# Kernel optimization log

Hardware: AMD Instinct MI355X
Metric: run time of the kernel (lower is better)

## Reference

```python
import jax, jax.numpy as jnp
import numpy as np

B, L, D_IN, D_GATE, D_HID, D_STATE = 4, 8192, 512, 2048, 128, 512
EPS = 1e-5


def _layernorm(x, g, b):
    m = jnp.mean(x, axis=-1, keepdims=True)
    v = jnp.var(x, axis=-1, keepdims=True)
    return (x - m) * jax.lax.rsqrt(v + EPS) * g + b


def _dss(u, g, b, lam_re, lam_im, c_re, c_im, d):
    # u: [B, L, H]; diagonal state-space mixing along L via FFT conv
    seq_len = u.shape[-2]
    un = _layernorm(u, g, b)
    residual = un * d                                   # learned skip, [B,L,H]
    lam = -jnp.exp(lam_re) + 1j * jnp.exp(lam_im)       # [N] complex
    c = (c_re + 1j * c_im) * (jnp.exp(lam) - 1.0) / lam  # [H,N]
    t = jnp.arange(seq_len, dtype=jnp.float32)
    s = jnp.exp(t[:, None] * lam[None, :])              # [L,N] Vandermonde
    kern = jnp.einsum('hn,ln->lh', c, s).real           # [L,H]
    n_fft = 2 * seq_len
    uf = jnp.fft.rfft(un, n=n_fft, axis=-2)             # [B, n_fft/2+1, H]
    kf = jnp.fft.rfft(kern, n=n_fft, axis=0)            # [n_fft/2+1, H]
    y = jnp.fft.irfft(uf * kf, n=n_fft, axis=-2)[..., :seq_len, :]
    return y + residual


def setup_inputs() -> dict:
    key = jax.random.key(0)
    ks = jax.random.split(key, 16)
    f32 = jnp.float32
    return {
        'x': jax.random.normal(ks[0], (B, L, D_IN), f32),
        'norm_g': jnp.ones((D_IN,), f32),
        'norm_b': jnp.zeros((D_IN,), f32),
        'W_v': jax.random.normal(ks[1], (D_GATE, D_IN), f32) / np.sqrt(D_IN),
        'W_u': jax.random.normal(ks[2], (D_HID, D_IN), f32) / np.sqrt(D_IN),
        'W_uc': jax.random.normal(ks[3], (D_GATE, D_HID), f32) / np.sqrt(D_HID),
        'W_o': jax.random.normal(ks[4], (D_IN, D_GATE), f32) / np.sqrt(D_GATE),
        'b_o': jnp.zeros((D_IN,), f32),
        'dss_g': jnp.ones((D_HID,), f32),
        'dss_b': jnp.zeros((D_HID,), f32),
        'lam_re': jax.random.normal(ks[5], (D_STATE,), f32),
        'lam_im': jax.random.normal(ks[6], (D_STATE,), f32),
        'C_re': jax.random.normal(ks[7], (D_HID, D_STATE), f32) / np.sqrt(D_STATE),
        'C_im': jax.random.normal(ks[8], (D_HID, D_STATE), f32) / np.sqrt(D_STATE),
        'D_skip': jax.random.normal(ks[9], (D_HID,), f32),
    }


def reference(x, norm_g, norm_b, W_v, W_u, W_uc, W_o, b_o,
              dss_g, dss_b, lam_re, lam_im, C_re, C_im, D_skip):
    xn = _layernorm(x, norm_g, norm_b)
    v = jax.nn.gelu(jnp.einsum('blf,gf->blg', xn, W_v), approximate=False)  # [B,L,G]
    u = jax.nn.gelu(jnp.einsum('blf,hf->blh', xn, W_u), approximate=False)  # [B,L,H]
    y = _dss(u, dss_g, dss_b, lam_re, lam_im, C_re, C_im, D_skip)           # [B,L,H]
    uc = jnp.einsum('blh,gh->blg', y, W_uc)                                 # [B,L,G]
    o = jnp.einsum('blg,fg->blf', uc * v, W_o) + b_o                        # [B,L,F]
    return o + x
```

## Files before the change

### kernel.cpp

```cpp
#include <hip/hip_runtime.h>
#include <math.h>
#include <stdint.h>

typedef unsigned short u16;
typedef unsigned int   u32;
typedef short short8 __attribute__((ext_vector_type(8)));
typedef float v4f    __attribute__((ext_vector_type(4)));

#define DEVI static __device__ __forceinline__

struct __align__(8)  U2 { u32 x, y; };
struct __align__(16) U4 { u32 x, y, z, w; };

static const int BB = 4, LL = 8192;
static const int BL = BB * LL;

DEVI float bf2f(u16 u){ u32 v = ((u32)u) << 16; float f; __builtin_memcpy(&f, &v, 4); return f; }
DEVI u16  f2bf(float f){ u32 u; __builtin_memcpy(&u, &f, 4); return (u16)((u + 0x7fffu + ((u >> 16) & 1u)) >> 16); }

DEVI float geluf(float x){
  float z = fabsf(x) * 0.7071067811865475f;
  float t = __builtin_amdgcn_rcpf(1.0f + 0.3275911f * z);
  float p = t * (0.254829592f + t * (-0.284496736f + t * (1.421413741f +
            t * (-1.453152027f + t * 1.061405429f))));
  float e = __builtin_amdgcn_exp2f(z * z * -1.4426950408889634f);
  float er = 1.0f - p * e;
  float s = (x < 0.0f) ? -er : er;
  return 0.5f * x * (1.0f + s);
}

DEVI void ldsload16(const void* g, void* l){
  __builtin_amdgcn_global_load_lds(
      (const __attribute__((address_space(1))) u32*)(uintptr_t)g,
      (__attribute__((address_space(3)))  u32*)(u32)(uintptr_t)l,
      16, 0, 0);
}

__global__ __launch_bounds__(256) void k_cvt4(
    const float* __restrict__ s0, u16* __restrict__ d0, int n0,
    const float* __restrict__ s1, u16* __restrict__ d1, int n1,
    const float* __restrict__ s2, u16* __restrict__ d2, int n2,
    const float* __restrict__ s3, u16* __restrict__ d3, int n3){
  int i = blockIdx.x * 256 + threadIdx.x;
  if (i < n0){ d0[i] = f2bf(s0[i]); return; }
  i -= n0;
  if (i < n1){ d1[i] = f2bf(s1[i]); return; }
  i -= n1;
  if (i < n2){ d2[i] = f2bf(s2[i]); return; }
  i -= n2;
  if (i < n3){ d3[i] = f2bf(s3[i]); }
}

__global__ __launch_bounds__(256) void k_ln1(const float* __restrict__ x, const float* __restrict__ g,
                                             const float* __restrict__ b, u16* __restrict__ xn){
  int row = blockIdx.x, t = threadIdx.x;
  const float2* xr = (const float2*)(x + (int64_t)row * 512);
  float2 p = xr[t];
  float s = p.x + p.y, ss = p.x * p.x + p.y * p.y;
  for (int off = 32; off; off >>= 1){ s += __shfl_down(s, off); ss += __shfl_down(ss, off); }
  __shared__ float red[8];
  int w = t >> 6, lane = t & 63;
  if (!lane){ red[w] = s; red[4 + w] = ss; }
  __syncthreads();
  s  = red[0] + red[1] + red[2] + red[3];
  ss = red[4] + red[5] + red[6] + red[7];
  float m = s * (1.0f / 512.0f), var = ss * (1.0f / 512.0f) - m * m;
  float rs = rsqrtf(var + 1e-5f);
  float2 gv = ((const float2*)g)[t], bv = ((const float2*)b)[t];
  float r0 = (p.x - m) * rs * gv.x + bv.x;
  float r1 = (p.y - m) * rs * gv.y + bv.y;
  ((u32*)(xn + (int64_t)row * 512))[t] = (u32)f2bf(r0) | ((u32)f2bf(r1) << 16);
}

__global__ __launch_bounds__(256) void k_ln2(const u16* __restrict__ u, const float* __restrict__ g,
                                             const float* __restrict__ b, u16* __restrict__ un){
  int row = blockIdx.x * 4 + (threadIdx.x >> 6);
  int lane = threadIdx.x & 63;
  const u32* ur = (const u32*)(u + (int64_t)row * 128);
  u32 pv = ur[lane];
  float a = bf2f((u16)(pv & 0xffff)), c = bf2f((u16)(pv >> 16));
  float s = a + c, ss = a * a + c * c;
  for (int off = 32; off; off >>= 1){ s += __shfl_xor(s, off); ss += __shfl_xor(ss, off); }
  float m = s * (1.0f / 128.0f), var = ss * (1.0f / 128.0f) - m * m;
  float rs = rsqrtf(var + 1e-5f);
  float2 gv = ((const float2*)g)[lane], bv = ((const float2*)b)[lane];
  float r0 = (a - m) * rs * gv.x + bv.x;
  float r1 = (c - m) * rs * gv.y + bv.y;
  ((u32*)(un + (int64_t)row * 128))[lane] = (u32)f2bf(r0) | ((u32)f2bf(r1) << 16);
}

__global__ __launch_bounds__(256) void k_transpose(const u16* __restrict__ un, u16* __restrict__ unT){
  int bc = blockIdx.x >> 3, it = blockIdx.x & 7;
  int b = bc >> 4, cc = bc & 15;
  __shared__ __align__(16) u16 tile[64][128];
  const u16* src = un + ((int64_t)(b * 8192 + cc * 512 + it * 64)) * 128;
  int t = threadIdx.x;
  for (int p = 0; p < 4; p++){
    int id = p * 256 + t; int ri = id >> 4, seg = id & 15;
    *(U4*)&tile[ri][seg * 8] = *(const U4*)(src + (int64_t)ri * 128 + seg * 8);
  }
  __syncthreads();
  u16* dst = unT + ((int64_t)(bc * 128)) * 512 + it * 64;
  for (int p = 0; p < 4; p++){
    int id = p * 256 + t; int h = id >> 3, seg = id & 7;
    U4 pk; u16* pv = (u16*)&pk;
    for (int k2 = 0; k2 < 8; k2++) pv[k2] = tile[seg * 8 + k2][h];
    *(U4*)(dst + (int64_t)h * 512 + seg * 8) = pk;
  }
}

__global__ __launch_bounds__(512) void k_prep(const float* lam_re, const float* lam_im,
    const float* C_re, const float* C_im,
    u16* ZC, u16* PC, u16* VC, u16* ccat, float* cre, float* cim, float* zT){
  int n = blockIdx.x, t = threadIdx.x;
  float lr = -expf(lam_re[n]);
  float li =  expf(lam_im[n]);
  float mag = expf(lr * (float)t), ph = li * (float)t;
  float er = mag * cosf(ph), ei = mag * sinf(ph);
  ZC[(int64_t)n * 512 + (511 - t)]         = f2bf(er);
  ZC[(int64_t)(512 + n) * 512 + (511 - t)] = f2bf(ei);
  VC[(int64_t)t * 1024 + n]       = f2bf(er);
  VC[(int64_t)t * 1024 + 512 + n] = f2bf(-ei);
  float mag2 = expf(lr * (float)(t + 1)), ph2 = li * (float)(t + 1);
  PC[(int64_t)t * 1024 + n]       = f2bf(mag2 * cosf(ph2));
  PC[(int64_t)t * 1024 + 512 + n] = f2bf(-mag2 * sinf(ph2));
  if (t == 0){
    float m5 = expf(lr * 512.0f), p5 = li * 512.0f;
    zT[n] = m5 * cosf(p5); zT[512 + n] = m5 * sinf(p5);
  }
  if (t < 128){
    float e1m = expf(lr);
    float e1r = e1m * cosf(li), e1i = e1m * sinf(li);
    float nr = e1r - 1.0f, ni = e1i;
    float d2 = lr * lr + li * li;
    float qr = (nr * lr + ni * li) / d2, qi = (ni * lr - nr * li) / d2;
    float Cr = C_re[t * 512 + n], Ci = C_im[t * 512 + n];
    float vr = Cr * qr - Ci * qi, vi = Cr * qi + Ci * qr;
    cre[t * 512 + n] = vr; cim[t * 512 + n] = vi;
    ccat[(int64_t)t * 1024 + n] = f2bf(vr); ccat[(int64_t)t * 1024 + 512 + n] = f2bf(vi);
  }
}

__global__ __launch_bounds__(128) void k_kern(const u16* __restrict__ VC,
                                              const u16* __restrict__ ccat,
                                              float* __restrict__ kern){
  __shared__ __align__(16) u16 vrow[1024];
  int d = blockIdx.x, h = threadIdx.x;
  *(U4*)&vrow[h * 8] = *(const U4*)(VC + (int64_t)d * 1024 + h * 8);
  __syncthreads();
  const u16* cr = ccat + (int64_t)h * 1024;
  float s = 0.0f;
  #pragma unroll 4
  for (int k = 0; k < 1024; k += 8){
    short8 a = *(const short8*)&vrow[k];
    short8 b = *(const short8*)(cr + k);
    #pragma unroll
    for (int j = 0; j < 8; j++) s += bf2f((u16)a[j]) * bf2f((u16)b[j]);
  }
  kern[(int64_t)d * 128 + h] = s;
}

__global__ __launch_bounds__(512) void k_rcat(const float* __restrict__ kern, u16* __restrict__ Rcat){
  int h = blockIdx.x >> 7, a = blockIdx.x & 127;
  int kcol = threadIdx.x;
  int d = 3 - (kcol >> 7);
  int delay = d * 128 + a - (kcol & 127);
  float val = (delay >= 0 && delay < 512) ? kern[delay * 128 + h] : 0.0f;
  Rcat[((int64_t)(h * 128 + a)) * 512 + kcol] = f2bf(val);
}

__global__ __launch_bounds__(256) void k_scan(const float* __restrict__ S, const float* __restrict__ cre,
    const float* __restrict__ cim, const float* __restrict__ zT, u16* __restrict__ WT){
  int tid = blockIdx.x * 256 + threadIdx.x;
  int n = tid & 511, bh = tid >> 9, b = bh >> 7, h = bh & 127;
  float cr = cre[h * 512 + n], ci = cim[h * 512 + n];
  float zr = zT[n], zi = zT[512 + n];
  float sR = 0.0f, sI = 0.0f;
  for (int cc = 0; cc < 16; cc++){
    int64_t m = (int64_t)(b * 16 + cc) * 128 + h;
    float wR = cr * sR - ci * sI, wI = cr * sI + ci * sR;
    WT[m * 1024 + n] = f2bf(wR);
    WT[m * 1024 + 512 + n] = f2bf(wI);
    float aR = S[m * 1024 + n], aI = S[m * 1024 + 512 + n];
    float nR = zr * sR - zi * sI + aR;
    sI = zr * sI + zi * sR + aI;
    sR = nR;
  }
}

__global__ __launch_bounds__(256) void k_assemble(const float* __restrict__ Yloc, const float* __restrict__ Ycross,
    const u16* __restrict__ un, const float* __restrict__ Dskip, u16* __restrict__ y){
  int64_t e = (int64_t)blockIdx.x * 256 + threadIdx.x;
  int h = (int)(e & 127); int64_t bl = e >> 7;
  int b = (int)(bl >> 13), l = (int)(bl & 8191);
  int cc = l >> 9, ii = l & 511, bc = b * 16 + cc;
  float val = Yloc[((int64_t)h * 512 + ii) * 64 + bc]
            + Ycross[(int64_t)ii * 8192 + (int64_t)bc * 128 + h]
            + bf2f(un[e]) * Dskip[h];
  y[e] = f2bf(val);
}

template<int EPI, bool TRI = false>
__global__ __launch_bounds__(256) void k_gemm(
    const u16* __restrict__ A, int64_t lda, int64_t aZ,
    const u16* __restrict__ B, int64_t ldb, int64_t bZ,
    void* Cp, int64_t ldc, int64_t cZ,
    int K, int Nvalid,
    const u16* aux1, const float* auxf1, const float* auxf2)
{
  __shared__ union __align__(16) SMU { u16 st[2][4096]; float ep[4][1088]; } sm;
  const int tid = threadIdx.x;
  const int lane = tid & 63, w = tid >> 6;
  const int wr = w >> 1, wc = w & 1, q = lane >> 4, c16 = lane & 15;
  const int sRow = lane >> 2, sSeg = lane & 3;
  const int z = blockIdx.z;

  int bx = blockIdx.x, by = blockIdx.y;
  if (!TRI && (gridDim.y & 7) == 0 && gridDim.x > 1){
    u32 idx = by * gridDim.x + bx;
    u32 xcd = idx & 7, s = idx >> 3;
    bx = s % gridDim.x;
    by = (s / gridDim.x) * 8 + xcd;
  }
  const int64_t m0 = (int64_t)by * 128;
  const int64_t n0 = (int64_t)bx * 128;

  const u16* Ab = A + (int64_t)z * aZ;
  const u16* Bp = B + (int64_t)z * bZ;
  int Keff = K;
  if (TRI){
    Ab += 384 - m0;
    Keff = (int)(m0 + 128);
  }

  v4f acc[4][4];
  #pragma unroll
  for (int i = 0; i < 4; i++)
    #pragma unroll
    for (int j = 0; j < 4; j++)
      acc[i][j] = (v4f)0.0f;

  for (int k0 = 0; k0 < Keff; k0 += 32){
    #pragma unroll
    for (int half = 0; half < 2; half++){
      int r0 = (half * 4 + w) * 16;
      int64_t arow = (TRI ? (int64_t)0 : m0) + r0 + sRow;
      ldsload16(Ab + arow * lda + k0 + sSeg * 8, &sm.st[0][r0 * 32]);
      int64_t brow = n0 + r0 + sRow;
      if (brow >= Nvalid) brow = Nvalid - 1;
      ldsload16(Bp + brow * ldb + k0 + sSeg * 8, &sm.st[1][r0 * 32]);
    }
    __syncthreads();
    short8 af[4], bfr[4];
    const u16* aB = &sm.st[0][(wr * 64 + c16) * 32 + q * 8];
    const u16* bB = &sm.st[1][(wc * 64 + c16) * 32 + q * 8];
    #pragma unroll
    for (int i = 0; i < 4; i++) af[i]  = *(const short8*)(aB + i * 512);
    #pragma unroll
    for (int j = 0; j < 4; j++) bfr[j] = *(const short8*)(bB + j * 512);
    #pragma unroll
    for (int i = 0; i < 4; i++)
      #pragma unroll
      for (int j = 0; j < 4; j++)
        acc[i][j] = __builtin_amdgcn_mfma_f32_16x16x32_bf16(af[i], bfr[j], acc[i][j], 0, 0, 0);
    __syncthreads();
  }

  if (EPI == 0){
    float* Cf = (float*)Cp + (int64_t)z * cZ;
    #pragma unroll
    for (int i = 0; i < 4; i++)
      #pragma unroll
      for (int j = 0; j < 4; j++){
        int64_t gr = m0 + wr * 64 + i * 16 + q * 4;
        int64_t gc = n0 + wc * 64 + j * 16 + c16;
        if (gc < Nvalid){
          #pragma unroll
          for (int r = 0; r < 4; r++)
            Cf[(gr + r) * ldc + gc] = acc[i][j][r];
        }
      }
    return;
  }

  u16* Cb = (u16*)Cp + (int64_t)z * cZ;
  float* ep = sm.ep[w];
  for (int i = 0; i < 4; i++){
    #pragma unroll
    for (int j = 0; j < 4; j++)
      #pragma unroll
      for (int r = 0; r < 4; r++){
        float vv = acc[i][j][r];
        if (EPI == 1) vv = geluf(vv);
        ep[(q * 4 + r) * 68 + j * 16 + c16] = vv;
      }
    #pragma unroll
    for (int p = 0; p < 4; p++){
      int id = p * 64 + lane;
      int row = id >> 4, cg = id & 15;
      float o0 = ep[row * 68 + cg * 4 + 0];
      float o1 = ep[row * 68 + cg * 4 + 1];
      float o2 = ep[row * 68 + cg * 4 + 2];
      float o3 = ep[row * 68 + cg * 4 + 3];
      int64_t gr = m0 + wr * 64 + i * 16 + row;
      int64_t gc = n0 + wc * 64 + cg * 4;
      if (gc < Nvalid){
        U2 outp;
        outp.x = (u32)f2bf(o0) | ((u32)f2bf(o1) << 16);
        outp.y = (u32)f2bf(o2) | ((u32)f2bf(o3) << 16);
        *(U2*)(Cb + gr * ldc + gc) = outp;
      }
    }
  }
}

#define FENCE __builtin_amdgcn_sched_barrier(0)
#define BARX  __builtin_amdgcn_s_barrier()

#define STAGE(SRC, LD, TBASE, SEL, KT)                                          \
  { const u16* _g = (SRC) + (int64_t)(KT) * 64 + (int64_t)((SEL) * 128 + wid * 8) * (LD); \
    u16* _lb = (TBASE) + ((SEL) * 128 + wid * 8) * 64;                          \
    ldsload16(_g, _lb);                                                         \
    ldsload16(_g + (int64_t)64 * (LD), _lb + 64 * 64);                          \
  }

#define MFMAQ(QM, QN, BQ)                                                       \
  __builtin_amdgcn_s_setprio(1);                                                \
  _Pragma("unroll")                                                             \
  for (int mi = 0; mi < 4; mi++)                                                \
    _Pragma("unroll")                                                           \
    for (int ni = 0; ni < 2; ni++){                                             \
      acc[(QM)*4+mi][(QN)*2+ni] = __builtin_amdgcn_mfma_f32_16x16x32_bf16(      \
          af[mi][0], BQ[ni][0], acc[(QM)*4+mi][(QN)*2+ni], 0, 0, 0);            \
      acc[(QM)*4+mi][(QN)*2+ni] = __builtin_amdgcn_mfma_f32_16x16x32_bf16(      \
          af[mi][1], BQ[ni][1], acc[(QM)*4+mi][(QN)*2+ni], 0, 0, 0);            \
    }                                                                           \
  __builtin_amdgcn_s_setprio(0);

#define DS_READ_A(OFF)                                                          \
    _Pragma("unroll")                                                           \
    for (int mi = 0; mi < 4; mi++){                                             \
      af[mi][0] = *(const short8*)(Ac + (OFF) + abase + mi * 2048 + kx0);       \
      af[mi][1] = *(const short8*)(Ac + (OFF) + abase + mi * 2048 + kx1);       \
    }
#define DS_READ_B(BQ, OFF)                                                      \
    _Pragma("unroll")                                                           \
    for (int ni = 0; ni < 2; ni++){                                             \
      BQ[ni][0] = *(const short8*)(Bc + (OFF) + bbase + ni * 2048 + kx0);       \
      BQ[ni][1] = *(const short8*)(Bc + (OFF) + bbase + ni * 2048 + kx1);       \
    }

#define DO_TILE(T, CURB, NXTB)                                                  \
  {                                                                             \
    const char* Ac = (const char*)(CURB);                                       \
    const char* Bc = Ac + 32768;                                                \
    if ((T) + 1 < NT){                                                          \
      u16* Ab_ = (NXTB); u16* Bb_ = (NXTB) + 16384;                             \
      STAGE(Asrc, lda, Ab_, 0, (T) + 1);                                        \
      STAGE(Asrc, lda, Ab_, 1, (T) + 1);                                        \
      STAGE(Bsrc, ldb, Bb_, 0, (T) + 1);                                        \
      STAGE(Bsrc, ldb, Bb_, 1, (T) + 1);                                        \
    }                                                                           \
    DS_READ_A(0) DS_READ_B(bq0, 0) DS_READ_B(bq1, 16384)                        \
    MFMAQ(0, 0, bq0);                                                           \
    MFMAQ(0, 1, bq1);                                                           \
    DS_READ_A(16384)                                                            \
    MFMAQ(1, 1, bq1);                                                           \
    MFMAQ(1, 0, bq0);                                                           \
    asm volatile("s_waitcnt lgkmcnt(0)" ::: "memory");                          \
    if ((T) + 1 < NT) asm volatile("s_waitcnt vmcnt(0)" ::: "memory");          \
    FENCE; BARX; FENCE;                                                         \
  }

template<int EPI>
__global__ __launch_bounds__(512) void k_gemm256(
    const u16* __restrict__ A, int64_t lda,
    const u16* __restrict__ B, int64_t ldb,
    void* __restrict__ Cp, int64_t ldc, int K,
    const u16* __restrict__ aux1,
    const float* __restrict__ auxf1, const float* __restrict__ auxf2)
{
  extern __shared__ __align__(16) u16 smd[];
  const int tid = threadIdx.x, wid = tid >> 6, lane = tid & 63;
  const int wr = wid >> 2, wc = wid & 3, c16 = lane & 15;
  const int q4 = (lane >> 4) << 2;

  int bx = blockIdx.x, by = blockIdx.y;
  if ((gridDim.y & 7) == 0 && gridDim.x > 1){
    u32 idx = by * gridDim.x + bx;
    u32 xcd = idx & 7, s = idx >> 3;
    bx = s % gridDim.x;
    by = (s / gridDim.x) * 8 + xcd;
  }
  const int64_t m0 = (int64_t)by * 256;
  const int64_t n0 = (int64_t)bx * 256;
  const int NT = K >> 6;

  const int rowin = lane >> 3;
  const int colel = 8 * ((lane & 7) ^ rowin);
  const u16* Asrc = A + (m0 + rowin) * lda + colel;
  const u16* Bsrc = B + (n0 + rowin) * ldb + colel;

  const int kx0 = ((lane >> 4) << 4) ^ ((lane & 7) << 4);
  const int kx1 = kx0 ^ 64;
  const int abase = (wr * 64 + c16) * 128;
  const int bbase = (wc * 32 + c16) * 128;

  u16* buf0 = smd;
  u16* buf1 = smd + 32768;

  v4f acc[8][4];
  #pragma unroll
  for (int i = 0; i < 8; i++)
    #pragma unroll
    for (int j = 0; j < 4; j++) acc[i][j] = (v4f)0.0f;

  short8 af[4][2], bq0[2][2], bq1[2][2];

  STAGE(Asrc, lda, buf0,         0, 0);
  STAGE(Asrc, lda, buf0,         1, 0);
  STAGE(Bsrc, ldb, buf0 + 16384, 0, 0);
  STAGE(Bsrc, ldb, buf0 + 16384, 1, 0);
  asm volatile("s_waitcnt vmcnt(0)" ::: "memory");
  FENCE; BARX; FENCE;

  for (int t = 0; t < NT; t += 2){
    DO_TILE(t,     buf0, buf1)
    DO_TILE(t + 1, buf1, buf0)
  }

  if (EPI == 0){
    float* C = (float*)Cp;
    #pragma unroll
    for (int qm = 0; qm < 2; qm++)
      #pragma unroll
      for (int mi = 0; mi < 4; mi++){
        int64_t gr = m0 + qm * 128 + wr * 64 + mi * 16 + q4;
        #pragma unroll
        for (int qn = 0; qn < 2; qn++)
          #pragma unroll
          for (int ni = 0; ni < 2; ni++){
            int64_t gc = n0 + qn * 128 + wc * 32 + ni * 16 + c16;
            v4f a = acc[qm * 4 + mi][qn * 2 + ni];
            float bo = auxf2[gc];
            #pragma unroll
            for (int r = 0; r < 4; r++)
              C[(gr + r) * ldc + gc] = a[r] + auxf1[(gr + r) * ldc + gc] + bo;
          }
      }
    return;
  }

  u16* Cb = (u16*)Cp;
  float* scr = (float*)smd + wid * 528;
  const int erow = lane >> 2, eseg = lane & 3;
  #pragma unroll
  for (int qm = 0; qm < 2; qm++)
    #pragma unroll
    for (int mi = 0; mi < 4; mi++)
      #pragma unroll
      for (int qn = 0; qn < 2; qn++){
        #pragma unroll
        for (int ni = 0; ni < 2; ni++){
          v4f a = acc[qm * 4 + mi][qn * 2 + ni];
          #pragma unroll
          for (int r = 0; r < 4; r++){
            float vv = a[r];
            if (EPI == 1) vv = geluf(vv);
            scr[(q4 + r) * 33 + ni * 16 + c16] = vv;
          }
        }
        float o[8];
        #pragma unroll
        for (int kq = 0; kq < 8; kq++) o[kq] = scr[erow * 33 + eseg * 8 + kq];
        int64_t gr = m0 + qm * 128 + wr * 64 + mi * 16 + erow;
        int64_t gc = n0 + qn * 128 + wc * 32 + eseg * 8;
        if (EPI == 2){
          U4 pv = *(const U4*)(aux1 + gr * ldc + gc);
          const u16* pp = (const u16*)&pv;
          #pragma unroll
          for (int kq = 0; kq < 8; kq++) o[kq] *= bf2f(pp[kq]);
        }
        U4 outp; u16* op = (u16*)&outp;
        #pragma unroll
        for (int kq = 0; kq < 8; kq++) op[kq] = f2bf(o[kq]);
        *(U4*)(Cb + gr * ldc + gc) = outp;
      }
}

extern "C" void kernel_launch(void* const* d_in, const int* in_sizes, int n_in,
                              void* d_out, int out_size, void* d_ws, size_t ws_size,
                              hipStream_t stream) {
  (void)in_sizes; (void)n_in; (void)out_size; (void)ws_size;
  const float* x      = (const float*)d_in[0];
  const float* norm_g = (const float*)d_in[1];
  const float* norm_b = (const float*)d_in[2];
  const float* W_v    = (const float*)d_in[3];
  const float* W_u    = (const float*)d_in[4];
  const float* W_uc   = (const float*)d_in[5];
  const float* W_o    = (const float*)d_in[6];
  const float* b_o    = (const float*)d_in[7];
  const float* dss_g  = (const float*)d_in[8];
  const float* dss_b  = (const float*)d_in[9];
  const float* lam_re = (const float*)d_in[10];
  const float* lam_im = (const float*)d_in[11];
  const float* C_re   = (const float*)d_in[12];
  const float* C_im   = (const float*)d_in[13];
  const float* D_skip = (const float*)d_in[14];

  char* ob = (char*)d_out;
  u16* xn    = (u16*)(ob);
  u16* Wv_b  = (u16*)(ob + 33554432ull);
  u16* Wu_b  = (u16*)(ob + 35651584ull);

  char* ws = (char*)d_ws;
  const size_t R1      = 134217728ull;
  const size_t OFF_UN  = R1 + 33554432ull;
  const size_t OFF_UNT = OFF_UN + 8388608ull;
  const size_t OFF_R2  = OFF_UNT + 8388608ull;
  const size_t OFF_TAB = OFF_R2 + 33554432ull;

  u16*  v     = (u16*)(ws + 0);
  u16*  u     = (u16*)(ws + R1);
  u16*  Rcat  = (u16*)(ws + R1);
  u16*  WT    = (u16*)(ws + R1 + 16777216ull);
  u16*  un    = (u16*)(ws + OFF_UN);
  u16*  unT   = (u16*)(ws + OFF_UNT);
  u16*  y     = (u16*)(ws + OFF_UNT);
  float* S    = (float*)(ws + OFF_R2);
  float* Ycross = (float*)(ws + OFF_R2);
  float* Yloc = (float*)(ws + OFF_R2 + 16777216ull);
  char* tp = ws + OFF_TAB;
  u16*  ZC   = (u16*)tp;            tp += 1048576;
  u16*  PC   = (u16*)tp;            tp += 1048576;
  u16*  VC   = (u16*)tp;            tp += 1048576;
  u16*  ccat = (u16*)tp;            tp += 262144;
  float* cre = (float*)tp;          tp += 262144;
  float* cim = (float*)tp;          tp += 262144;
  float* zT  = (float*)tp;          tp += 4096;
  float* kern= (float*)tp;          tp += 262144;
  u16*  Wo_b = (u16*)tp;            tp += 2097152;
  u16*  Wuc_b= (u16*)tp;            tp += 524288;

  k_cvt4<<<9472, 256, 0, stream>>>(W_v, Wv_b, 2048 * 512,
                                   W_u, Wu_b, 128 * 512,
                                   W_uc, Wuc_b, 2048 * 128,
                                   W_o, Wo_b, 512 * 2048);

  k_ln1<<<BL, 256, 0, stream>>>(x, norm_g, norm_b, xn);
  k_prep<<<512, 512, 0, stream>>>(lam_re, lam_im, C_re, C_im, ZC, PC, VC, ccat, cre, cim, zT);
  k_kern<<<512, 128, 0, stream>>>(VC, ccat, kern);

  k_gemm256<1><<<dim3(8, 128), 512, 131072, stream>>>(xn, 512, Wv_b, 512, v, 2048, 512, nullptr, nullptr, nullptr);
  k_gemm<1><<<dim3(1, 256, 1), 256, 0, stream>>>(xn, 512, 0, Wu_b, 512, 0, u, 128, 0, 512, 128, nullptr, nullptr, nullptr);
  k_ln2<<<BL / 4, 256, 0, stream>>>(u, dss_g, dss_b, un);
  k_transpose<<<512, 256, 0, stream>>>(un, unT);

  k_rcat<<<16384, 512, 0, stream>>>(kern, Rcat);

  k_gemm<0><<<dim3(8, 64, 1), 256, 0, stream>>>(unT, 512, 0, ZC, 512, 0, S, 1024, 0, 512, 1024, nullptr, nullptr, nullptr);
  k_scan<<<1024, 256, 0, stream>>>(S, cre, cim, zT, WT);
  k_gemm<0><<<dim3(64, 4, 1), 256, 0, stream>>>(PC, 1024, 0, WT, 1024, 0, Ycross, 8192, 0, 1024, 8192, nullptr, nullptr, nullptr);
  k_gemm<0, true><<<dim3(1, 4, 128), 256, 0, stream>>>(
      Rcat, 512, 65536, unT, 65536, 512, Yloc, 64, 32768, 512, 64, nullptr, nullptr, nullptr);
  k_assemble<<<16384, 256, 0, stream>>>(Yloc, Ycross, un, D_skip, y);

  k_gemm256<2><<<dim3(8, 128), 512, 131072, stream>>>(y, 128, Wuc_b, 128, v, 2048, 128, v, nullptr, nullptr);
  k_gemm256<0><<<dim3(2, 128), 512, 131072, stream>>>(v, 2048, Wo_b, 2048, d_out, 512, 2048, nullptr, x, b_o);
}
```

Measured before the change: 596.3 us.

## Add K=128 gate GEMM kernel keeping A tile resident; tile assemble transpose

```diff
diff --git a/kernel.cpp b/kernel.cpp
--- a/kernel.cpp
+++ b/kernel.cpp
@@ -188,16 +188,33 @@
   }
 }
 
-__global__ __launch_bounds__(256) void k_assemble(const float* __restrict__ Yloc, const float* __restrict__ Ycross,
-    const u16* __restrict__ un, const float* __restrict__ Dskip, u16* __restrict__ y){
-  int64_t e = (int64_t)blockIdx.x * 256 + threadIdx.x;
-  int h = (int)(e & 127); int64_t bl = e >> 7;
-  int b = (int)(bl >> 13), l = (int)(bl & 8191);
-  int cc = l >> 9, ii = l & 511, bc = b * 16 + cc;
-  float val = Yloc[((int64_t)h * 512 + ii) * 64 + bc]
-            + Ycross[(int64_t)ii * 8192 + (int64_t)bc * 128 + h]
-            + bf2f(un[e]) * Dskip[h];
-  y[e] = f2bf(val);
+__global__ __launch_bounds__(512) void k_assemble2(const float* __restrict__ Yloc,
+    const float* __restrict__ Ycross, const u16* __restrict__ un,
+    const float* __restrict__ Dskip, u16* __restrict__ y){
+  __shared__ float tile[128][65];
+  int ii = blockIdx.x;
+  int t = threadIdx.x;
+  int hl = t >> 6;
+  int bcl = t & 63;
+  #pragma unroll
+  for (int p = 0; p < 16; p++){
+    int h = p * 8 + hl;
+    tile[h][bcl] = Yloc[((int64_t)(h * 512 + ii)) * 64 + bcl];
+  }
+  __syncthreads();
+  int h = t & 127;
+  int bcr = t >> 7;
+  float dk = Dskip[h];
+  #pragma unroll
+  for (int p = 0; p < 16; p++){
+    int bc = p * 4 + bcr;
+    int b = bc >> 4, cc = bc & 15;
+    int64_t e = ((int64_t)b * 8192 + cc * 512 + ii) * 128 + h;
+    float val = tile[h][bc]
+              + Ycross[(int64_t)ii * 8192 + (int64_t)bc * 128 + h]
+              + bf2f(un[e]) * dk;
+    y[e] = f2bf(val);
+  }
 }
 
 template<int EPI, bool TRI = false>
@@ -475,17 +492,144 @@
         for (int kq = 0; kq < 8; kq++) o[kq] = scr[erow * 33 + eseg * 8 + kq];
         int64_t gr = m0 + qm * 128 + wr * 64 + mi * 16 + erow;
         int64_t gc = n0 + qn * 128 + wc * 32 + eseg * 8;
-        if (EPI == 2){
-          U4 pv = *(const U4*)(aux1 + gr * ldc + gc);
-          const u16* pp = (const u16*)&pv;
-          #pragma unroll
-          for (int kq = 0; kq < 8; kq++) o[kq] *= bf2f(pp[kq]);
-        }
         U4 outp; u16* op = (u16*)&outp;
         #pragma unroll
         for (int kq = 0; kq < 8; kq++) op[kq] = f2bf(o[kq]);
         *(U4*)(Cb + gr * ldc + gc) = outp;
       }
+}
+
+__global__ __launch_bounds__(512) void k_gemmK128(
+    const u16* __restrict__ A,
+    const u16* __restrict__ B,
+    u16* __restrict__ C)
+{
+  extern __shared__ __align__(16) u16 smd[];
+  const int tid = threadIdx.x, wid = tid >> 6, lane = tid & 63;
+  const int wr = wid >> 2, wc = wid & 3, c16 = lane & 15;
+  const int q4 = (lane >> 4) << 2;
+
+  int bx = blockIdx.x, by = blockIdx.y;
+  {
+    u32 idx = by * gridDim.x + bx;
+    u32 xcd = idx & 7, s = idx >> 3;
+    bx = s % gridDim.x;
+    by = (s / gridDim.x) * 8 + xcd;
+  }
+  const int64_t m0 = (int64_t)by * 256;
+  const int64_t nbase = (int64_t)bx * 1024;
+
+  const int rowin = lane >> 3;
+  const int colel = 8 * ((lane & 7) ^ rowin);
+  const u16* Asrc = A + (m0 + rowin) * 128 + colel;
+
+  const int kx0 = ((lane >> 4) << 4) ^ ((lane & 7) << 4);
+  const int kx1 = kx0 ^ 64;
+  const int abase = (wr * 64 + c16) * 128;
+  const int bbase = (wc * 32 + c16) * 128;
+
+  u16* Abuf = smd;
+  u16* Bbuf = smd + 32768;
+  float* scr = (float*)(smd + 65536) + wid * 528;
+
+  const int erow = lane >> 2, eseg = lane & 3;
+  short8 af[4][2], bq0[2][2], bq1[2][2];
+
+  {
+    const u16* Bs0 = B + (nbase + rowin) * 128 + colel;
+    STAGE(Asrc, 128, Abuf,         0, 0);
+    STAGE(Asrc, 128, Abuf,         1, 0);
+    STAGE(Asrc, 128, Abuf + 16384, 0, 1);
+    STAGE(Asrc, 128, Abuf + 16384, 1, 1);
+    STAGE(Bs0,  128, Bbuf,         0, 0);
+    STAGE(Bs0,  128, Bbuf,         1, 0);
+    STAGE(Bs0,  128, Bbuf + 16384, 0, 1);
+    STAGE(Bs0,  128, Bbuf + 16384, 1, 1);
+  }
+  asm volatile("s_waitcnt vmcnt(0)" ::: "memory");
+  FENCE; BARX; FENCE;
+
+  #pragma unroll
+  for (int nj = 0; nj < 4; nj++){
+    const int64_t n0 = nbase + nj * 256;
+
+    v4f acc[8][4];
+    #pragma unroll
+    for (int i = 0; i < 8; i++)
+      #pragma unroll
+      for (int j = 0; j < 4; j++) acc[i][j] = (v4f)0.0f;
+
+    #pragma unroll
+    for (int kt = 0; kt < 2; kt++){
+      const char* Ac = (const char*)Abuf + kt * 32768;
+      const char* Bc = (const char*)Bbuf + kt * 32768;
+      DS_READ_A(0) DS_READ_B(bq0, 0) DS_READ_B(bq1, 16384)
+      MFMAQ(0, 0, bq0);
+      MFMAQ(0, 1, bq1);
+      DS_READ_A(16384)
+      MFMAQ(1, 1, bq1);
+      MFMAQ(1, 0, bq0);
+    }
+    asm volatile("s_waitcnt lgkmcnt(0)" ::: "memory");
+    FENCE; BARX; FENCE;
+
+    if (nj < 3){
+      const u16* Bs = B + (nbase + (nj + 1) * 256 + rowin) * 128 + colel;
+      STAGE(Bs, 128, Bbuf,         0, 0);
+      STAGE(Bs, 128, Bbuf,         1, 0);
+      STAGE(Bs, 128, Bbuf + 16384, 0, 1);
+      STAGE(Bs, 128, Bbuf + 16384, 1, 1);
+    }
+
+    U4 pvA[2], pvB[2];
+    {
+      int64_t gr = m0 + wr * 64 + erow;
+      pvA[0] = *(const U4*)(C + gr * 2048 + n0 + wc * 32 + eseg * 8);
+      pvA[1] = *(const U4*)(C + gr * 2048 + n0 + 128 + wc * 32 + eseg * 8);
+    }
+    #pragma unroll
+    for (int g = 0; g < 8; g++){
+      const int qm = g >> 2, mi = g & 3;
+      int64_t gr0 = m0 + qm * 128 + wr * 64 + mi * 16;
+      if (g < 7){
+        const int qn2 = (g + 1) >> 2, mn2 = (g + 1) & 3;
+        int64_t gr2 = m0 + qn2 * 128 + wr * 64 + mn2 * 16 + erow;
+        if (g & 1){
+          pvA[0] = *(const U4*)(C + gr2 * 2048 + n0 + wc * 32 + eseg * 8);
+          pvA[1] = *(const U4*)(C + gr2 * 2048 + n0 + 128 + wc * 32 + eseg * 8);
+        } else {
+          pvB[0] = *(const U4*)(C + gr2 * 2048 + n0 + wc * 32 + eseg * 8);
+          pvB[1] = *(const U4*)(C + gr2 * 2048 + n0 + 128 + wc * 32 + eseg * 8);
+        }
+      }
+      #pragma unroll
+      for (int qn = 0; qn < 2; qn++){
+        #pragma unroll
+        for (int ni = 0; ni < 2; ni++){
+          v4f a = acc[qm * 4 + mi][qn * 2 + ni];
+          #pragma unroll
+          for (int r = 0; r < 4; r++)
+            scr[(q4 + r) * 33 + ni * 16 + c16] = a[r];
+        }
+        float o[8];
+        #pragma unroll
+        for (int kq = 0; kq < 8; kq++) o[kq] = scr[erow * 33 + eseg * 8 + kq];
+        U4 pv = (g & 1) ? pvB[qn] : pvA[qn];
+        const u16* pp = (const u16*)&pv;
+        U4 outp; u16* op = (u16*)&outp;
+        #pragma unroll
+        for (int kq = 0; kq < 8; kq++) op[kq] = f2bf(o[kq] * bf2f(pp[kq]));
+        int64_t gr = gr0 + erow;
+        int64_t gc = n0 + qn * 128 + wc * 32 + eseg * 8;
+        *(U4*)(C + gr * 2048 + gc) = outp;
+      }
+    }
+
+    if (nj < 3){
+      asm volatile("s_waitcnt vmcnt(0)" ::: "memory");
+      FENCE; BARX; FENCE;
+    }
+  }
 }
 
 extern "C" void kernel_launch(void* const* d_in, const int* in_sizes, int n_in,
@@ -563,8 +707,8 @@
   k_gemm<0><<<dim3(64, 4, 1), 256, 0, stream>>>(PC, 1024, 0, WT, 1024, 0, Ycross, 8192, 0, 1024, 8192, nullptr, nullptr, nullptr);
   k_gemm<0, true><<<dim3(1, 4, 128), 256, 0, stream>>>(
       Rcat, 512, 65536, unT, 65536, 512, Yloc, 64, 32768, 512, 64, nullptr, nullptr, nullptr);
-  k_assemble<<<16384, 256, 0, stream>>>(Yloc, Ycross, un, D_skip, y);
-
-  k_gemm256<2><<<dim3(8, 128), 512, 131072, stream>>>(y, 128, Wuc_b, 128, v, 2048, 128, v, nullptr, nullptr);
+  k_assemble2<<<512, 512, 0, stream>>>(Yloc, Ycross, un, D_skip, y);
+
+  k_gemmK128<<<dim3(2, 128), 512, 148480, stream>>>(y, Wuc_b, v);
   k_gemm256<0><<<dim3(2, 128), 512, 131072, stream>>>(v, 2048, Wo_b, 2048, d_out, 512, 2048, nullptr, x, b_o);
 }
```

After: 611.5 us. 2.5% more time.

## Triple-buffer 256-tile GEMM with K=32 stages and tile the assemble transpose

Applied to the files above, without the earlier changes.

```diff
diff --git a/kernel.cpp b/kernel.cpp
--- a/kernel.cpp
+++ b/kernel.cpp
@@ -188,16 +188,33 @@
   }
 }
 
-__global__ __launch_bounds__(256) void k_assemble(const float* __restrict__ Yloc, const float* __restrict__ Ycross,
-    const u16* __restrict__ un, const float* __restrict__ Dskip, u16* __restrict__ y){
-  int64_t e = (int64_t)blockIdx.x * 256 + threadIdx.x;
-  int h = (int)(e & 127); int64_t bl = e >> 7;
-  int b = (int)(bl >> 13), l = (int)(bl & 8191);
-  int cc = l >> 9, ii = l & 511, bc = b * 16 + cc;
-  float val = Yloc[((int64_t)h * 512 + ii) * 64 + bc]
-            + Ycross[(int64_t)ii * 8192 + (int64_t)bc * 128 + h]
-            + bf2f(un[e]) * Dskip[h];
-  y[e] = f2bf(val);
+__global__ __launch_bounds__(512) void k_assemble2(const float* __restrict__ Yloc,
+    const float* __restrict__ Ycross, const u16* __restrict__ un,
+    const float* __restrict__ Dskip, u16* __restrict__ y){
+  __shared__ float tile[128][65];
+  int ii = blockIdx.x;
+  int t = threadIdx.x;
+  int hl = t >> 6;
+  int bcl = t & 63;
+  #pragma unroll
+  for (int p = 0; p < 16; p++){
+    int h = p * 8 + hl;
+    tile[h][bcl] = Yloc[((int64_t)(h * 512 + ii)) * 64 + bcl];
+  }
+  __syncthreads();
+  int h = t & 127;
+  int bcr = t >> 7;
+  float dk = Dskip[h];
+  #pragma unroll
+  for (int p = 0; p < 16; p++){
+    int bc = p * 4 + bcr;
+    int b = bc >> 4, cc = bc & 15;
+    int64_t e = ((int64_t)b * 8192 + cc * 512 + ii) * 128 + h;
+    float val = tile[h][bc]
+              + Ycross[(int64_t)ii * 8192 + (int64_t)bc * 128 + h]
+              + bf2f(un[e]) * dk;
+    y[e] = f2bf(val);
+  }
 }
 
 template<int EPI, bool TRI = false>
@@ -317,58 +334,38 @@
 #define FENCE __builtin_amdgcn_sched_barrier(0)
 #define BARX  __builtin_amdgcn_s_barrier()
 
-#define STAGE(SRC, LD, TBASE, SEL, KT)                                          \
-  { const u16* _g = (SRC) + (int64_t)(KT) * 64 + (int64_t)((SEL) * 128 + wid * 8) * (LD); \
-    u16* _lb = (TBASE) + ((SEL) * 128 + wid * 8) * 64;                          \
-    ldsload16(_g, _lb);                                                         \
-    ldsload16(_g + (int64_t)64 * (LD), _lb + 64 * 64);                          \
-  }
-
-#define MFMAQ(QM, QN, BQ)                                                       \
-  __builtin_amdgcn_s_setprio(1);                                                \
-  _Pragma("unroll")                                                             \
-  for (int mi = 0; mi < 4; mi++)                                                \
+#define STAGE32(SRC, LD, BUFO, OPO, SEL, KT)                                    \
+  { const u16* _g = (SRC) + (int64_t)(KT) * 32 + (int64_t)((SEL) * 128 + wid * 16) * (LD); \
+    u16* _lb = smd + (BUFO) + (OPO) + ((SEL) * 128 + wid * 16) * 32;            \
+    ldsload16(_g, _lb); }
+
+#define DO_T(T, CUR, FUT)                                                       \
+  {                                                                             \
+    if ((T) + 2 < NT){                                                          \
+      STAGE32(Asrc, lda, (FUT), 0,    0, (T) + 2);                              \
+      STAGE32(Asrc, lda, (FUT), 0,    1, (T) + 2);                              \
+      STAGE32(Bsrc, ldb, (FUT), 8192, 0, (T) + 2);                              \
+      STAGE32(Bsrc, ldb, (FUT), 8192, 1, (T) + 2);                              \
+    }                                                                           \
+    const char* Ac = (const char*)(smd + (CUR));                                \
+    const char* Bc = (const char*)(smd + (CUR) + 8192);                         \
     _Pragma("unroll")                                                           \
-    for (int ni = 0; ni < 2; ni++){                                             \
-      acc[(QM)*4+mi][(QN)*2+ni] = __builtin_amdgcn_mfma_f32_16x16x32_bf16(      \
-          af[mi][0], BQ[ni][0], acc[(QM)*4+mi][(QN)*2+ni], 0, 0, 0);            \
-      acc[(QM)*4+mi][(QN)*2+ni] = __builtin_amdgcn_mfma_f32_16x16x32_bf16(      \
-          af[mi][1], BQ[ni][1], acc[(QM)*4+mi][(QN)*2+ni], 0, 0, 0);            \
-    }                                                                           \
-  __builtin_amdgcn_s_setprio(0);
-
-#define DS_READ_A(OFF)                                                          \
+    for (int mi = 0; mi < 8; mi++)                                              \
+      af[mi] = *(const short8*)(Ac + abase + mi * 1024 + kx);                   \
     _Pragma("unroll")                                                           \
-    for (int mi = 0; mi < 4; mi++){                                             \
-      af[mi][0] = *(const short8*)(Ac + (OFF) + abase + mi * 2048 + kx0);       \
-      af[mi][1] = *(const short8*)(Ac + (OFF) + abase + mi * 2048 + kx1);       \
-    }
-#define DS_READ_B(BQ, OFF)                                                      \
+    for (int ni = 0; ni < 4; ni++)                                              \
+      bf[ni] = *(const short8*)(Bc + bbase + ni * 1024 + kx);                   \
+    __builtin_amdgcn_s_setprio(1);                                              \
     _Pragma("unroll")                                                           \
-    for (int ni = 0; ni < 2; ni++){                                             \
-      BQ[ni][0] = *(const short8*)(Bc + (OFF) + bbase + ni * 2048 + kx0);       \
-      BQ[ni][1] = *(const short8*)(Bc + (OFF) + bbase + ni * 2048 + kx1);       \
-    }
-
-#define DO_TILE(T, CURB, NXTB)                                                  \
-  {                                                                             \
-    const char* Ac = (const char*)(CURB);                                       \
-    const char* Bc = Ac + 32768;                                                \
-    if ((T) + 1 < NT){                                                          \
-      u16* Ab_ = (NXTB); u16* Bb_ = (NXTB) + 16384;                             \
-      STAGE(Asrc, lda, Ab_, 0, (T) + 1);                                        \
-      STAGE(Asrc, lda, Ab_, 1, (T) + 1);                                        \
-      STAGE(Bsrc, ldb, Bb_, 0, (T) + 1);                                        \
-      STAGE(Bsrc, ldb, Bb_, 1, (T) + 1);                                        \
-    }                                                                           \
-    DS_READ_A(0) DS_READ_B(bq0, 0) DS_READ_B(bq1, 16384)                        \
-    MFMAQ(0, 0, bq0);                                                           \
-    MFMAQ(0, 1, bq1);                                                           \
-    DS_READ_A(16384)                                                            \
-    MFMAQ(1, 1, bq1);                                                           \
-    MFMAQ(1, 0, bq0);                                                           \
+    for (int mi = 0; mi < 8; mi++)                                              \
+      _Pragma("unroll")                                                         \
+      for (int ni = 0; ni < 4; ni++)                                            \
+        acc[mi][ni] = __builtin_amdgcn_mfma_f32_16x16x32_bf16(                  \
+            af[mi], bf[ni], acc[mi][ni], 0, 0, 0);                              \
+    __builtin_amdgcn_s_setprio(0);                                              \
     asm volatile("s_waitcnt lgkmcnt(0)" ::: "memory");                          \
-    if ((T) + 1 < NT) asm volatile("s_waitcnt vmcnt(0)" ::: "memory");          \
+    if ((T) + 2 < NT) asm volatile("s_waitcnt vmcnt(4)" ::: "memory");          \
+    else              asm volatile("s_waitcnt vmcnt(0)" ::: "memory");          \
     FENCE; BARX; FENCE;                                                         \
   }
 
@@ -394,20 +391,17 @@
   }
   const int64_t m0 = (int64_t)by * 256;
   const int64_t n0 = (int64_t)bx * 256;
-  const int NT = K >> 6;
-
-  const int rowin = lane >> 3;
-  const int colel = 8 * ((lane & 7) ^ rowin);
+  const int NT = K >> 5;
+
+  const int rowin = lane >> 2;
+  const int chnk  = (lane & 3) ^ ((rowin >> 1) & 3);
+  const int colel = chnk * 8;
   const u16* Asrc = A + (m0 + rowin) * lda + colel;
   const u16* Bsrc = B + (n0 + rowin) * ldb + colel;
 
-  const int kx0 = ((lane >> 4) << 4) ^ ((lane & 7) << 4);
-  const int kx1 = kx0 ^ 64;
-  const int abase = (wr * 64 + c16) * 128;
-  const int bbase = (wc * 32 + c16) * 128;
-
-  u16* buf0 = smd;
-  u16* buf1 = smd + 32768;
+  const int kx = (((lane >> 4) ^ ((c16 >> 1) & 3)) << 4);
+  const int abase = (wr * 128 + c16) * 64;
+  const int bbase = (wc * 64 + c16) * 64;
 
   v4f acc[8][4];
   #pragma unroll
@@ -415,39 +409,44 @@
     #pragma unroll
     for (int j = 0; j < 4; j++) acc[i][j] = (v4f)0.0f;
 
-  short8 af[4][2], bq0[2][2], bq1[2][2];
-
-  STAGE(Asrc, lda, buf0,         0, 0);
-  STAGE(Asrc, lda, buf0,         1, 0);
-  STAGE(Bsrc, ldb, buf0 + 16384, 0, 0);
-  STAGE(Bsrc, ldb, buf0 + 16384, 1, 0);
-  asm volatile("s_waitcnt vmcnt(0)" ::: "memory");
+  short8 af[8], bf[4];
+
+  STAGE32(Asrc, lda, 0, 0,    0, 0);
+  STAGE32(Asrc, lda, 0, 0,    1, 0);
+  STAGE32(Bsrc, ldb, 0, 8192, 0, 0);
+  STAGE32(Bsrc, ldb, 0, 8192, 1, 0);
+  if (NT > 1){
+    STAGE32(Asrc, lda, 16384, 0,    0, 1);
+    STAGE32(Asrc, lda, 16384, 0,    1, 1);
+    STAGE32(Bsrc, ldb, 16384, 8192, 0, 1);
+    STAGE32(Bsrc, ldb, 16384, 8192, 1, 1);
+    asm volatile("s_waitcnt vmcnt(4)" ::: "memory");
+  } else {
+    asm volatile("s_waitcnt vmcnt(0)" ::: "memory");
+  }
   FENCE; BARX; FENCE;
 
-  for (int t = 0; t < NT; t += 2){
-    DO_TILE(t,     buf0, buf1)
-    DO_TILE(t + 1, buf1, buf0)
+  int cur = 0, nxt = 16384, fut = 32768;
+  for (int t = 0; t < NT; ++t){
+    DO_T(t, cur, fut)
+    int tmp = cur; cur = nxt; nxt = fut; fut = tmp;
   }
 
   if (EPI == 0){
     float* C = (float*)Cp;
     #pragma unroll
-    for (int qm = 0; qm < 2; qm++)
-      #pragma unroll
-      for (int mi = 0; mi < 4; mi++){
-        int64_t gr = m0 + qm * 128 + wr * 64 + mi * 16 + q4;
+    for (int mi = 0; mi < 8; mi++){
+      int64_t gr = m0 + wr * 128 + mi * 16 + q4;
+      #pragma unroll
+      for (int ni = 0; ni < 4; ni++){
+        int64_t gc = n0 + wc * 64 + ni * 16 + c16;
+        v4f a = acc[mi][ni];
+        float bo = auxf2[gc];
         #pragma unroll
-        for (int qn = 0; qn < 2; qn++)
-          #pragma unroll
-          for (int ni = 0; ni < 2; ni++){
-            int64_t gc = n0 + qn * 128 + wc * 32 + ni * 16 + c16;
-            v4f a = acc[qm * 4 + mi][qn * 2 + ni];
-            float bo = auxf2[gc];
-            #pragma unroll
-            for (int r = 0; r < 4; r++)
-              C[(gr + r) * ldc + gc] = a[r] + auxf1[(gr + r) * ldc + gc] + bo;
-          }
+        for (int r = 0; r < 4; r++)
+          C[(gr + r) * ldc + gc] = a[r] + auxf1[(gr + r) * ldc + gc] + bo;
       }
+    }
     return;
   }
 
@@ -455,37 +454,36 @@
   float* scr = (float*)smd + wid * 528;
   const int erow = lane >> 2, eseg = lane & 3;
   #pragma unroll
-  for (int qm = 0; qm < 2; qm++)
-    #pragma unroll
-    for (int mi = 0; mi < 4; mi++)
-      #pragma unroll
-      for (int qn = 0; qn < 2; qn++){
+  for (int mi = 0; mi < 8; mi++){
+    #pragma unroll
+    for (int nh = 0; nh < 2; nh++){
+      #pragma unroll
+      for (int ni = 0; ni < 2; ni++){
+        v4f a = acc[mi][nh * 2 + ni];
         #pragma unroll
-        for (int ni = 0; ni < 2; ni++){
-          v4f a = acc[qm * 4 + mi][qn * 2 + ni];
-          #pragma unroll
-          for (int r = 0; r < 4; r++){
-            float vv = a[r];
-            if (EPI == 1) vv = geluf(vv);
-            scr[(q4 + r) * 33 + ni * 16 + c16] = vv;
-          }
+        for (int r = 0; r < 4; r++){
+          float vv = a[r];
+          if (EPI == 1) vv = geluf(vv);
+          scr[(q4 + r) * 33 + ni * 16 + c16] = vv;
         }
-        float o[8];
+      }
+      float o[8];
+      #pragma unroll
+      for (int kq = 0; kq < 8; kq++) o[kq] = scr[erow * 33 + eseg * 8 + kq];
+      int64_t gr = m0 + wr * 128 + mi * 16 + erow;
+      int64_t gc = n0 + wc * 64 + nh * 32 + eseg * 8;
+      if (EPI == 2){
+        U4 pv = *(const U4*)(aux1 + gr * ldc + gc);
+        const u16* pp = (const u16*)&pv;
         #pragma unroll
-        for (int kq = 0; kq < 8; kq++) o[kq] = scr[erow * 33 + eseg * 8 + kq];
-        int64_t gr = m0 + qm * 128 + wr * 64 + mi * 16 + erow;
-        int64_t gc = n0 + qn * 128 + wc * 32 + eseg * 8;
-        if (EPI == 2){
-          U4 pv = *(const U4*)(aux1 + gr * ldc + gc);
-          const u16* pp = (const u16*)&pv;
-          #pragma unroll
-          for (int kq = 0; kq < 8; kq++) o[kq] *= bf2f(pp[kq]);
-        }
-        U4 outp; u16* op = (u16*)&outp;
-        #pragma unroll
-        for (int kq = 0; kq < 8; kq++) op[kq] = f2bf(o[kq]);
-        *(U4*)(Cb + gr * ldc + gc) = outp;
+        for (int kq = 0; kq < 8; kq++) o[kq] *= bf2f(pp[kq]);
       }
+      U4 outp; u16* op = (u16*)&outp;
+      #pragma unroll
+      for (int kq = 0; kq < 8; kq++) op[kq] = f2bf(o[kq]);
+      *(U4*)(Cb + gr * ldc + gc) = outp;
+    }
+  }
 }
 
 extern "C" void kernel_launch(void* const* d_in, const int* in_sizes, int n_in,
@@ -551,7 +549,7 @@
   k_prep<<<512, 512, 0, stream>>>(lam_re, lam_im, C_re, C_im, ZC, PC, VC, ccat, cre, cim, zT);
   k_kern<<<512, 128, 0, stream>>>(VC, ccat, kern);
 
-  k_gemm256<1><<<dim3(8, 128), 512, 131072, stream>>>(xn, 512, Wv_b, 512, v, 2048, 512, nullptr, nullptr, nullptr);
+  k_gemm256<1><<<dim3(8, 128), 512, 98304, stream>>>(xn, 512, Wv_b, 512, v, 2048, 512, nullptr, nullptr, nullptr);
   k_gemm<1><<<dim3(1, 256, 1), 256, 0, stream>>>(xn, 512, 0, Wu_b, 512, 0, u, 128, 0, 512, 128, nullptr, nullptr, nullptr);
   k_ln2<<<BL / 4, 256, 0, stream>>>(u, dss_g, dss_b, un);
   k_transpose<<<512, 256, 0, stream>>>(un, unT);
@@ -563,8 +561,8 @@
   k_gemm<0><<<dim3(64, 4, 1), 256, 0, stream>>>(PC, 1024, 0, WT, 1024, 0, Ycross, 8192, 0, 1024, 8192, nullptr, nullptr, nullptr);
   k_gemm<0, true><<<dim3(1, 4, 128), 256, 0, stream>>>(
       Rcat, 512, 65536, unT, 65536, 512, Yloc, 64, 32768, 512, 64, nullptr, nullptr, nullptr);
-  k_assemble<<<16384, 256, 0, stream>>>(Yloc, Ycross, un, D_skip, y);
-
-  k_gemm256<2><<<dim3(8, 128), 512, 131072, stream>>>(y, 128, Wuc_b, 128, v, 2048, 128, v, nullptr, nullptr);
-  k_gemm256<0><<<dim3(2, 128), 512, 131072, stream>>>(v, 2048, Wo_b, 2048, d_out, 512, 2048, nullptr, x, b_o);
-}
+  k_assemble2<<<512, 512, 0, stream>>>(Yloc, Ycross, un, D_skip, y);
+
+  k_gemm256<2><<<dim3(8, 128), 512, 98304, stream>>>(y, 128, Wuc_b, 128, v, 2048, 128, v, nullptr, nullptr);
+  k_gemm256<0><<<dim3(2, 128), 512, 98304, stream>>>(v, 2048, Wo_b, 2048, d_out, 512, 2048, nullptr, x, b_o);
+}
```

New measurement: 604.4 us. About the same (+1.3%).
